# Optimization experiments

Hardware: AMD Instinct MI355X
Metric: run time of the kernel (lower is better)

Reference implementation:

```python
import jax, jax.numpy as jnp
from jax import lax
import numpy as np

B = 512
IN_CAPS, OUT_CAPS, IN_DIM, OUT_DIM, ITERS = 32 * 6 * 6, 10, 8, 16, 3
EPS = 1e-8


def setup_inputs() -> dict:
    key = jax.random.key(0)
    ks = jax.random.split(key, 12)
    inp = {
        "x": jax.random.normal(ks[0], (B, 1, 28, 28), dtype=jnp.float32),
        "conv1_w": jax.random.normal(ks[1], (256, 1, 9, 9), dtype=jnp.float32) * 0.05,
        "conv1_b": jnp.zeros((256,), dtype=jnp.float32),
        "conv2_w": jax.random.normal(ks[2], (256, 256, 9, 9), dtype=jnp.float32) * 0.02,
        "conv2_b": jnp.zeros((256,), dtype=jnp.float32),
        "W": jax.random.normal(ks[3], (IN_CAPS, OUT_CAPS, IN_DIM, OUT_DIM), dtype=jnp.float32) * 0.1,
        "d1_w": jax.random.normal(ks[4], (OUT_DIM * OUT_CAPS, 512), dtype=jnp.float32) * 0.05,
        "d1_b": jnp.zeros((512,), dtype=jnp.float32),
        "d2_w": jax.random.normal(ks[5], (512, 1024), dtype=jnp.float32) * 0.05,
        "d2_b": jnp.zeros((1024,), dtype=jnp.float32),
        "d3_w": jax.random.normal(ks[6], (1024, 28 * 28), dtype=jnp.float32) * 0.05,
        "d3_b": jnp.zeros((28 * 28,), dtype=jnp.float32),
    }
    return inp


def _squash(s):
    # s2/(1+s2) * s/sqrt(s2+eps), norm over last dim
    s2 = jnp.sum(s * s, axis=-1, keepdims=True)
    return s2 / (1.0 + s2) * (s / jnp.sqrt(s2 + EPS))


def _conv(x, w, b, stride):
    y = lax.conv_general_dilated(x, w, (stride, stride), "VALID",
                                 dimension_numbers=("NCHW", "OIHW", "NCHW"))
    return y + b[None, :, None, None]


def reference(x, conv1_w, conv1_b, conv2_w, conv2_b, W,
              d1_w, d1_b, d2_w, d2_b, d3_w, d3_b):
    h = jax.nn.relu(_conv(x, conv1_w, conv1_b, 1))          # [B,256,20,20]
    h = _conv(h, conv2_w, conv2_b, 2)                       # [B,256,6,6]
    u = h.reshape(h.shape[0], 8, IN_CAPS).transpose(0, 2, 1)  # [B,1152,8]
    u = _squash(u)

    # dynamic routing
    u_hat = jnp.einsum("ijnm,bin->bijm", W, u)              # [B,1152,10,16]
    b_log = jnp.zeros((u.shape[0], IN_CAPS, OUT_CAPS), dtype=u.dtype)
    v = None
    for _ in range(ITERS):
        c = jax.nn.softmax(b_log, axis=1)                   # over in_capsules (as original)
        s = jnp.einsum("bij,bijm->bjm", c, u_hat)           # [B,10,16]
        v = _squash(s)
        b_log = b_log + jnp.einsum("bjm,bijm->bij", v, u_hat)
    caps = v                                                # [B,10,16]

    pred = jnp.argmax(jnp.sum(caps * caps, axis=-1), axis=-1)  # [B]
    mask = jax.lax.stop_gradient(jax.nn.one_hot(pred, OUT_CAPS, dtype=caps.dtype))
    dec_in = (caps * mask[:, :, None]).reshape(caps.shape[0], -1)  # [B,160]
    r = jax.nn.relu(dec_in @ d1_w + d1_b)
    r = jax.nn.relu(r @ d2_w + d2_b)
    r = jax.nn.sigmoid(r @ d3_w + d3_b)
    recon = r.reshape(-1, 1, 28, 28)
    return caps, recon, pred
```

## Files before the change

kernel.cpp:

```cpp
#include <hip/hip_runtime.h>

#define CAPS_EPS 1e-8f

typedef __attribute__((ext_vector_type(8))) short short8;
typedef __attribute__((ext_vector_type(4))) float f32x4;

__device__ inline ushort bf16_rn(float f) {
    uint u = __float_as_uint(f);
    u += 0x7fff + ((u >> 16) & 1);
    return (ushort)(u >> 16);
}
__device__ inline float bf16_f(ushort h) { return __uint_as_float((uint)h << 16); }

__device__ __forceinline__ void gld16(const void* g, void* l) {
    __builtin_amdgcn_global_load_lds(
        (const __attribute__((address_space(1))) unsigned int*)g,
        (__attribute__((address_space(3))) unsigned int*)l, 16, 0, 0);
}


__global__ __launch_bounds__(256) void k_pre(const float* __restrict__ w2,
                                             ushort* __restrict__ wBhi,
                                             ushort* __restrict__ wBlo,
                                             const float* __restrict__ x,
                                             ushort* __restrict__ xhi,
                                             ushort* __restrict__ xlo,
                                             const float* __restrict__ w1,
                                             ushort* __restrict__ w1phi,
                                             ushort* __restrict__ w1plo) {
    int bx = blockIdx.x, tid = threadIdx.x;
    if (bx < 256) {
        __shared__ float ld[81 * 65];
        int n = bx;
        const float* src = w2 + (size_t)n * 20736;
        for (int cc = 0; cc < 4; ++cc) {
            for (int i = tid; i < 5184; i += 256) {
                int c_loc = i / 81, t = i - c_loc * 81;
                ld[t * 65 + c_loc] = src[cc * 5184 + i];
            }
            __syncthreads();
            for (int i = tid; i < 5184; i += 256) {
                int t = i >> 6, c_loc = i & 63;
                float f = ld[t * 65 + c_loc];
                ushort hi = bf16_rn(f);
                ushort lo = bf16_rn(f - bf16_f(hi));
                size_t o = (size_t)n * 20736 + t * 256 + cc * 64 + c_loc;
                wBhi[o] = hi;
                wBlo[o] = lo;
            }
            __syncthreads();
        }
    } else if (bx < 256 + 1569) {
        int idx = (bx - 256) * 256 + tid;
        if (idx < 401408) {
            float f = x[idx];
            ushort hi = bf16_rn(f);
            ushort lo = bf16_rn(f - bf16_f(hi));
            xhi[idx] = hi;
            xlo[idx] = lo;
        } else if (idx < 401472) {
            xhi[idx] = 0;
            xlo[idx] = 0;
        }
    } else {
        int idx = (bx - 1825) * 256 + tid;
        int c = idx / 160;
        int kk160 = idx - c * 160;
        int kstep = kk160 >> 5, kk = kk160 & 31;
        int ky = kstep * 2 + (kk >> 4), kx = kk & 15;
        float f = (ky < 9 && kx < 9) ? w1[c * 81 + ky * 9 + kx] : 0.f;
        ushort hi = bf16_rn(f);
        ushort lo = bf16_rn(f - bf16_f(hi));
        w1phi[idx] = hi;
        w1plo[idx] = lo;
    }
}

__global__ __launch_bounds__(256) void k_conv1m(const ushort* __restrict__ xhi,
                                                const ushort* __restrict__ xlo,
                                                const ushort* __restrict__ w1phi,
                                                const ushort* __restrict__ w1plo,
                                                const float* __restrict__ b1,
                                                ushort* __restrict__ h1hi,
                                                ushort* __restrict__ h1lo) {
    int tid = threadIdx.x;
    int wv = tid >> 6, lane = tid & 63;
    int lrow = lane & 15, quad = lane >> 4;
    int m0 = blockIdx.x * 128 + wv * 32;
    int c0 = blockIdx.y * 64;

    int am[2];
#pragma unroll
    for (int t = 0; t < 2; ++t) {
        int m = m0 + t * 16 + lrow;
        int b = m / 400, r = m - b * 400;
        int y = r / 20, xx = r - y * 20;
        am[t] = b * 784 + y * 28 + xx;
    }

    f32x4 acc[2][4];
#pragma unroll
    for (int t = 0; t < 2; ++t)
#pragma unroll
        for (int tn = 0; tn < 4; ++tn) acc[t][tn] = (f32x4){0.f, 0.f, 0.f, 0.f};

    for (int kstep = 0; kstep < 5; ++kstep) {
        int arow = (kstep * 2 + (quad >> 1)) * 28 + (quad & 1) * 8;
        int boff = kstep * 32 + quad * 8;
        short8 bh[4], bl2[4];
#pragma unroll
        for (int tn = 0; tn < 4; ++tn) {
            int br = (c0 + tn * 16 + lrow) * 160 + boff;
            bh[tn] = *reinterpret_cast<const short8*>(w1phi + br);
            bl2[tn] = *reinterpret_cast<const short8*>(w1plo + br);
        }
#pragma unroll
        for (int t = 0; t < 2; ++t) {
            short8 ah = *reinterpret_cast<const short8*>(xhi + am[t] + arow);
            short8 al = *reinterpret_cast<const short8*>(xlo + am[t] + arow);
#pragma unroll
            for (int tn = 0; tn < 4; ++tn) {
                acc[t][tn] = __builtin_amdgcn_mfma_f32_16x16x32_bf16(ah, bh[tn], acc[t][tn], 0, 0, 0);
                acc[t][tn] = __builtin_amdgcn_mfma_f32_16x16x32_bf16(ah, bl2[tn], acc[t][tn], 0, 0, 0);
                acc[t][tn] = __builtin_amdgcn_mfma_f32_16x16x32_bf16(al, bh[tn], acc[t][tn], 0, 0, 0);
            }
        }
    }

#pragma unroll
    for (int t = 0; t < 2; ++t)
#pragma unroll
        for (int r = 0; r < 4; ++r) {
            int m = m0 + t * 16 + quad * 4 + r;
#pragma unroll
            for (int tn = 0; tn < 4; ++tn) {
                int c = c0 + tn * 16 + lrow;
                float v = acc[t][tn][r] + b1[c];
                v = fmaxf(v, 0.f);
                ushort hi = bf16_rn(v);
                ushort lo = bf16_rn(v - bf16_f(hi));
                h1hi[(size_t)m * 256 + c] = hi;
                h1lo[(size_t)m * 256 + c] = lo;
            }
        }
}

__global__ __launch_bounds__(256) void k_h2init4(const float* __restrict__ b2,
                                                 float* __restrict__ h2) {
    size_t idx = (size_t)blockIdx.x * 256 + threadIdx.x;
    const float4* b24 = reinterpret_cast<const float4*>(b2);
    reinterpret_cast<float4*>(h2)[idx] = b24[idx & 63];
}

__global__ __launch_bounds__(256, 2) void k_conv2m(const ushort* __restrict__ h1hi,
                                                   const ushort* __restrict__ h1lo,
                                                   const ushort* __restrict__ wBhi,
                                                   const ushort* __restrict__ wBlo,
                                                   float* __restrict__ h2) {
    __shared__ ushort Ahi[128 * 32];
    __shared__ ushort Alo[128 * 32];
    __shared__ ushort Bhi[256 * 32];
    __shared__ ushort Blo[256 * 32];
    int tid = threadIdx.x;
    int m0 = blockIdx.y * 128;
    int kbase = blockIdx.x * 2592;

    int wv = tid >> 6, lane = tid & 63;
    int cq = (lane & 3) * 8;

    int ra = wv * 32 + (lane >> 2);
    int mA0 = m0 + ra, mA1 = mA0 + 16;
    int mb0 = mA0 / 36, mp0 = mA0 - mb0 * 36;
    int mb1 = mA1 / 36, mp1 = mA1 - mb1 * 36;
    size_t a0 = ((size_t)mb0 * 400 + (mp0 / 6) * 40 + (mp0 % 6) * 2) * 256 + cq;
    size_t a1 = ((size_t)mb1 * 400 + (mp1 / 6) * 40 + (mp1 % 6) * 2) * 256 + cq;
    int ldsA = wv * 1024;

    int rb = wv * 64 + (lane >> 2);
    size_t bB = (size_t)rb * 20736 + cq;
    int ldsB = wv * 2048;

    int mhalf = (wv >> 1) * 64, nhalf = (wv & 1) * 128;
    int lrow = lane & 15, quad = lane >> 4;

    f32x4 acc[4][8];
#pragma unroll
    for (int a = 0; a < 4; ++a)
#pragma unroll
        for (int bq = 0; bq < 8; ++bq) acc[a][bq] = (f32x4){0.f, 0.f, 0.f, 0.f};

    for (int ks = 0; ks < 81; ++ks) {
        int k = kbase + ks * 32;
        int t = k >> 8, cc = k & 255;
        int ky = t / 9, kx = t - ky * 9;
        size_t koffA = (size_t)(ky * 5120 + kx * 256 + cc);

        __syncthreads();
        gld16(h1hi + a0 + koffA, &Ahi[ldsA]);
        gld16(h1hi + a1 + koffA, &Ahi[ldsA + 512]);
        gld16(h1lo + a0 + koffA, &Alo[ldsA]);
        gld16(h1lo + a1 + koffA, &Alo[ldsA + 512]);
#pragma unroll
        for (int q = 0; q < 4; ++q) {
            size_t bo = bB + (size_t)q * 331776 + k;
            gld16(wBhi + bo, &Bhi[ldsB + q * 512]);
            gld16(wBlo + bo, &Blo[ldsB + q * 512]);
        }
        __syncthreads();

        short8 ah[4], al[4];
#pragma unroll
        for (int tm = 0; tm < 4; ++tm) {
            int off = (mhalf + tm * 16 + lrow) * 32 + quad * 8;
            ah[tm] = *reinterpret_cast<short8*>(&Ahi[off]);
            al[tm] = *reinterpret_cast<short8*>(&Alo[off]);
        }
#pragma unroll
        for (int tn = 0; tn < 8; ++tn) {
            int off = (nhalf + tn * 16 + lrow) * 32 + quad * 8;
            short8 bh = *reinterpret_cast<short8*>(&Bhi[off]);
            short8 bl2 = *reinterpret_cast<short8*>(&Blo[off]);
#pragma unroll
            for (int tm = 0; tm < 4; ++tm) {
                acc[tm][tn] = __builtin_amdgcn_mfma_f32_16x16x32_bf16(ah[tm], bh, acc[tm][tn], 0, 0, 0);
                acc[tm][tn] = __builtin_amdgcn_mfma_f32_16x16x32_bf16(ah[tm], bl2, acc[tm][tn], 0, 0, 0);
                acc[tm][tn] = __builtin_amdgcn_mfma_f32_16x16x32_bf16(al[tm], bh, acc[tm][tn], 0, 0, 0);
            }
        }
    }

#pragma unroll
    for (int tm = 0; tm < 4; ++tm) {
        int mrow = m0 + mhalf + tm * 16 + quad * 4;
#pragma unroll
        for (int tn = 0; tn < 8; ++tn) {
            int ncol = nhalf + tn * 16 + lrow;
#pragma unroll
            for (int r = 0; r < 4; ++r)
                atomicAdd(&h2[(size_t)(mrow + r) * 256 + ncol], acc[tm][tn][r]);
        }
    }
}

__device__ __forceinline__ void wtrans(const float* __restrict__ src,
                                       ushort* __restrict__ dh,
                                       ushort* __restrict__ dl,
                                       float* ld, int kt, int nt, int K, int N,
                                       int tid) {
    for (int i = tid; i < 4096; i += 256) {
        int kk = i >> 6, nn = i & 63;
        int k = kt * 64 + kk, n = nt * 64 + nn;
        float f = (k < K && n < N) ? src[(size_t)k * N + n] : 0.f;
        ld[kk * 65 + nn] = f;
    }
    __syncthreads();
    for (int i = tid; i < 4096; i += 256) {
        int nn = i >> 6, kk = i & 63;
        int k = kt * 64 + kk, n = nt * 64 + nn;
        if (k < K) {
            float f = ld[kk * 65 + nn];
            ushort hi = bf16_rn(f);
            ushort lo = bf16_rn(f - bf16_f(hi));
            dh[(size_t)n * K + k] = hi;
            dl[(size_t)n * K + k] = lo;
        }
    }
}

__global__ __launch_bounds__(256) void k_post(const float* __restrict__ h2,
                                              float* __restrict__ uT,
                                              float* __restrict__ zr,
                                              const float* __restrict__ d1w,
                                              const float* __restrict__ d2w,
                                              const float* __restrict__ d3w,
                                              ushort* __restrict__ d1wThi, ushort* __restrict__ d1wTlo,
                                              ushort* __restrict__ d2wThi, ushort* __restrict__ d2wTlo,
                                              ushort* __restrict__ d3wThi, ushort* __restrict__ d3wTlo) {
    __shared__ float smem[8224 + 1056];
    int bx = blockIdx.x, t = threadIdx.x;
    if (bx < 576) {
        float (*ld)[257] = (float (*)[257])smem;
        float (*scl)[33] = (float (*)[33])(smem + 8224);
        int s = bx % 36;
        int b0 = (bx / 36) * 32;
        for (int bb = 0; bb < 32; ++bb)
            ld[bb][t] = h2[((size_t)(b0 + bb) * 36 + s) * 256 + t];
        __syncthreads();
        int b = t & 31, gb = (t >> 5) * 4;
#pragma unroll
        for (int q = 0; q < 4; ++q) {
            int g = gb + q;
            float s2 = 0.f;
#pragma unroll
            for (int n = 0; n < 8; ++n) {
                float vv = ld[b][g + n * 32];
                s2 = fmaf(vv, vv, s2);
            }
            scl[b][g] = s2 / ((1.f + s2) * sqrtf(s2 + CAPS_EPS));
        }
        __syncthreads();
        int hf = t >> 5;
        for (int gg = 0; gg < 32; ++gg) {
            int idx = hf * 32 + gg;
            int g = idx >> 3, n = idx & 7;
            uT[(((size_t)g * 36 + s) * 8 + n) * 512 + b0 + b] = ld[b][g + n * 32] * scl[b][g];
        }
    } else if (bx < 6421) {
        reinterpret_cast<float4*>(zr)[(size_t)(bx - 576) * 256 + t] = make_float4(0, 0, 0, 0);
    } else if (bx < 6445) {
        int local = bx - 6421;
        wtrans(d1w, d1wThi, d1wTlo, smem, local / 8, local % 8, 160, 512, t);
    } else if (bx < 6573) {
        int local = bx - 6445;
        wtrans(d2w, d2wThi, d2wTlo, smem, local / 16, local % 16, 512, 1024, t);
    } else {
        int local = bx - 6573;
        wtrans(d3w, d3wThi, d3wTlo, smem, local / 14, local % 14, 1024, 784, t);
    }
}

__global__ __launch_bounds__(256) void k_s(const float* __restrict__ Wc,
                                           const float* __restrict__ uT,
                                           const float* __restrict__ bl,
                                           const float* __restrict__ Z,
                                           float* __restrict__ sT,
                                           int first) {
    __shared__ float lw[8 * 1280];
    int tid = threadIdx.x;
    int i0 = blockIdx.x * 8;
    int b = blockIdx.y * 128 + (tid & 127);
    int mh = tid >> 7;
    const float* wg = Wc + (size_t)i0 * 1280;
#pragma unroll
    for (int r = 0; r < 10; ++r) {
        int q4 = (r * 256 + tid) * 4;
        *reinterpret_cast<float4*>(&lw[q4]) = *reinterpret_cast<const float4*>(wg + q4);
    }
    __syncthreads();
    float rzs[10];
    if (!first) {
#pragma unroll
        for (int j = 0; j < 10; ++j) rzs[j] = 1.0f / Z[j * 512 + b];
    }
    float acc[80];
#pragma unroll
    for (int q = 0; q < 80; ++q) acc[q] = 0.f;
    for (int di = 0; di < 8; ++di) {
        int i = i0 + di;
        float ur[8];
#pragma unroll
        for (int n = 0; n < 8; ++n) ur[n] = uT[((size_t)i * 8 + n) * 512 + b];
#pragma unroll
        for (int j = 0; j < 10; ++j) {
            float c;
            if (first) c = (1.0f / 1152.0f);
            else c = expf(bl[((size_t)i * 10 + j) * 512 + b]) * rzs[j];
            const float* wp = &lw[(di * 10 + j) * 128 + mh * 8];
            float4 s0 = {0.f, 0.f, 0.f, 0.f}, s1 = {0.f, 0.f, 0.f, 0.f};
#pragma unroll
            for (int n = 0; n < 8; ++n) {
                const float4* wq = reinterpret_cast<const float4*>(wp + n * 16);
                float4 wa = wq[0], wb = wq[1];
                float un = ur[n];
                s0.x = fmaf(un, wa.x, s0.x); s0.y = fmaf(un, wa.y, s0.y);
                s0.z = fmaf(un, wa.z, s0.z); s0.w = fmaf(un, wa.w, s0.w);
                s1.x = fmaf(un, wb.x, s1.x); s1.y = fmaf(un, wb.y, s1.y);
                s1.z = fmaf(un, wb.z, s1.z); s1.w = fmaf(un, wb.w, s1.w);
            }
            acc[j * 8 + 0] = fmaf(c, s0.x, acc[j * 8 + 0]);
            acc[j * 8 + 1] = fmaf(c, s0.y, acc[j * 8 + 1]);
            acc[j * 8 + 2] = fmaf(c, s0.z, acc[j * 8 + 2]);
            acc[j * 8 + 3] = fmaf(c, s0.w, acc[j * 8 + 3]);
            acc[j * 8 + 4] = fmaf(c, s1.x, acc[j * 8 + 4]);
            acc[j * 8 + 5] = fmaf(c, s1.y, acc[j * 8 + 5]);
            acc[j * 8 + 6] = fmaf(c, s1.z, acc[j * 8 + 6]);
            acc[j * 8 + 7] = fmaf(c, s1.w, acc[j * 8 + 7]);
        }
    }
#pragma unroll
    for (int j = 0; j < 10; ++j)
#pragma unroll
        for (int mm = 0; mm < 8; ++mm)
            atomicAdd(&sT[(j * 16 + mh * 8 + mm) * 512 + b], acc[j * 8 + mm]);
}

__global__ __launch_bounds__(256) void k_v(const float* __restrict__ sT,
                                           float* __restrict__ v,
                                           float* __restrict__ vT,
                                           float* __restrict__ sTz,
                                           float* __restrict__ Z) {
    int idx = blockIdx.x * 256 + threadIdx.x;
    int j = idx >> 9;
    int b = idx & 511;
    float sv[16];
    float s2 = 0.f;
#pragma unroll
    for (int m = 0; m < 16; ++m) {
        sv[m] = sT[(j * 16 + m) * 512 + b];
        s2 = fmaf(sv[m], sv[m], s2);
    }
    float scale = s2 / ((1.f + s2) * sqrtf(s2 + CAPS_EPS));
#pragma unroll
    for (int m = 0; m < 16; ++m) {
        float val = sv[m] * scale;
        v[(size_t)b * 160 + j * 16 + m] = val;
        vT[(j * 16 + m) * 512 + b] = val;
        sTz[(j * 16 + m) * 512 + b] = 0.f;
    }
    Z[idx] = 0.f;
}

__global__ __launch_bounds__(256) void k_bupd(const float* __restrict__ Wc,
                                              const float* __restrict__ uT,
                                              const float* __restrict__ vT,
                                              float* __restrict__ bl,
                                              float* __restrict__ Z) {
    __shared__ float lw[8 * 1280];
    int tid = threadIdx.x;
    int i0 = blockIdx.x * 8;
    int b = blockIdx.y * 128 + (tid & 127);
    int ih = tid >> 7;
    const float* wg = Wc + (size_t)i0 * 1280;
#pragma unroll
    for (int r = 0; r < 10; ++r) {
        int q4 = (r * 256 + tid) * 4;
        *reinterpret_cast<float4*>(&lw[q4]) = *reinterpret_cast<const float4*>(wg + q4);
    }
    __syncthreads();
    float ur[4][8];
#pragma unroll
    for (int ii = 0; ii < 4; ++ii) {
        int i = i0 + ih * 4 + ii;
#pragma unroll
        for (int n = 0; n < 8; ++n) ur[ii][n] = uT[((size_t)i * 8 + n) * 512 + b];
    }
    for (int j = 0; j < 10; ++j) {
        float vj[16];
#pragma unroll
        for (int m = 0; m < 16; ++m) vj[m] = vT[(j * 16 + m) * 512 + b];
        float zp = 0.f;
#pragma unroll
        for (int ii = 0; ii < 4; ++ii) {
            int di = ih * 4 + ii;
            const float* wp = &lw[(di * 10 + j) * 128];
            float t = 0.f;
#pragma unroll
            for (int n = 0; n < 8; ++n) {
                const float4* wq = reinterpret_cast<const float4*>(wp + n * 16);
                float4 w0 = wq[0], w1 = wq[1], w2 = wq[2], w3 = wq[3];
                float wvv = w0.x * vj[0];
                wvv = fmaf(w0.y, vj[1], wvv);  wvv = fmaf(w0.z, vj[2], wvv);
                wvv = fmaf(w0.w, vj[3], wvv);  wvv = fmaf(w1.x, vj[4], wvv);
                wvv = fmaf(w1.y, vj[5], wvv);  wvv = fmaf(w1.z, vj[6], wvv);
                wvv = fmaf(w1.w, vj[7], wvv);  wvv = fmaf(w2.x, vj[8], wvv);
                wvv = fmaf(w2.y, vj[9], wvv);  wvv = fmaf(w2.z, vj[10], wvv);
                wvv = fmaf(w2.w, vj[11], wvv); wvv = fmaf(w3.x, vj[12], wvv);
                wvv = fmaf(w3.y, vj[13], wvv); wvv = fmaf(w3.z, vj[14], wvv);
                wvv = fmaf(w3.w, vj[15], wvv);
                t = fmaf(ur[ii][n], wvv, t);
            }
            size_t idx = ((size_t)(i0 + di) * 10 + j) * 512 + b;
            float nb = bl[idx] + t;
            bl[idx] = nb;
            zp += expf(nb);
        }
        atomicAdd(&Z[j * 512 + b], zp);
    }
}

__global__ __launch_bounds__(256) void k_pred(const float* __restrict__ v,
                                              float* __restrict__ out,
                                              ushort* __restrict__ dechi,
                                              ushort* __restrict__ declo,
                                              int pred_off) {
    int b = blockIdx.x, t = threadIdx.x;
    __shared__ float sq[160];
    __shared__ float nrm[10];
    __shared__ int ip;
    float val = 0.f;
    if (t < 160) {
        val = v[(size_t)b * 160 + t];
        out[(size_t)b * 160 + t] = val;
        sq[t] = val * val;
    }
    __syncthreads();
    if (t < 10) {
        float s = 0.f;
#pragma unroll
        for (int k = 0; k < 16; ++k) s += sq[t * 16 + k];
        nrm[t] = s;
    }
    __syncthreads();
    if (t == 0) {
        float best = nrm[0];
        int bi = 0;
        for (int j = 1; j < 10; ++j)
            if (nrm[j] > best) { best = nrm[j]; bi = j; }
        ip = bi;
        out[(size_t)pred_off + b] = (float)bi;
    }
    __syncthreads();
    if (t < 160) {
        float d = ((t >> 4) == ip) ? val : 0.f;
        ushort hi = bf16_rn(d);
        ushort lo = bf16_rn(d - bf16_f(hi));
        dechi[(size_t)b * 160 + t] = hi;
        declo[(size_t)b * 160 + t] = lo;
    }
}

template <int ACT, int SPLIT_OUT>
__global__ __launch_bounds__(256) void k_gemmm(const ushort* __restrict__ Ahi,
                                               const ushort* __restrict__ Alo,
                                               const ushort* __restrict__ Bhi,
                                               const ushort* __restrict__ Blo,
                                               const float* __restrict__ bias,
                                               ushort* __restrict__ Chi,
                                               ushort* __restrict__ Clo,
                                               float* __restrict__ Cf,
                                               int K, int Ng) {
    int tid = threadIdx.x;
    int wv = tid >> 6, lane = tid & 63;
    int lrow = lane & 15, quad = lane >> 4;
    int m0 = blockIdx.x * 64 + (wv >> 1) * 32;
    int n0 = blockIdx.y * 128 + (wv & 1) * 64;

    f32x4 acc[2][4];
#pragma unroll
    for (int t = 0; t < 2; ++t)
#pragma unroll
        for (int tn = 0; tn < 4; ++tn) acc[t][tn] = (f32x4){0.f, 0.f, 0.f, 0.f};

    for (int ks = 0; ks < K; ks += 32) {
        int boff = ks + quad * 8;
        short8 bh[4], bl2[4];
#pragma unroll
        for (int tn = 0; tn < 4; ++tn) {
            size_t br = (size_t)(n0 + tn * 16 + lrow) * K + boff;
            bh[tn] = *reinterpret_cast<const short8*>(Bhi + br);
            bl2[tn] = *reinterpret_cast<const short8*>(Blo + br);
        }
#pragma unroll
        for (int t = 0; t < 2; ++t) {
            size_t ar = (size_t)(m0 + t * 16 + lrow) * K + boff;
            short8 ah = *reinterpret_cast<const short8*>(Ahi + ar);
            short8 al = *reinterpret_cast<const short8*>(Alo + ar);
#pragma unroll
            for (int tn = 0; tn < 4; ++tn) {
                acc[t][tn] = __builtin_amdgcn_mfma_f32_16x16x32_bf16(ah, bh[tn], acc[t][tn], 0, 0, 0);
                acc[t][tn] = __builtin_amdgcn_mfma_f32_16x16x32_bf16(ah, bl2[tn], acc[t][tn], 0, 0, 0);
                acc[t][tn] = __builtin_amdgcn_mfma_f32_16x16x32_bf16(al, bh[tn], acc[t][tn], 0, 0, 0);
            }
        }
    }

#pragma unroll
    for (int t = 0; t < 2; ++t)
#pragma unroll
        for (int r = 0; r < 4; ++r) {
            int m = m0 + t * 16 + quad * 4 + r;
#pragma unroll
            for (int tn = 0; tn < 4; ++tn) {
                int n = n0 + tn * 16 + lrow;
                if (n < Ng) {
                    float val = acc[t][tn][r] + bias[n];
                    if (ACT == 0) val = fmaxf(val, 0.f);
                    else val = 1.f / (1.f + expf(-val));
                    if (SPLIT_OUT) {
                        ushort hi = bf16_rn(val);
                        ushort lo = bf16_rn(val - bf16_f(hi));
                        Chi[(size_t)m * Ng + n] = hi;
                        Clo[(size_t)m * Ng + n] = lo;
                    } else {
                        Cf[(size_t)m * Ng + n] = val;
                    }
                }
            }
        }
}

extern "C" void kernel_launch(void* const* d_in, const int* in_sizes, int n_in,
                              void* d_out, int out_size, void* d_ws, size_t ws_size,
                              hipStream_t stream) {
    const float* x   = (const float*)d_in[0];
    const float* w1  = (const float*)d_in[1];
    const float* b1  = (const float*)d_in[2];
    const float* w2  = (const float*)d_in[3];
    const float* b2  = (const float*)d_in[4];
    const float* Wc  = (const float*)d_in[5];
    const float* d1w = (const float*)d_in[6];
    const float* d1b = (const float*)d_in[7];
    const float* d2w = (const float*)d_in[8];
    const float* d2b = (const float*)d_in[9];
    const float* d3w = (const float*)d_in[10];
    const float* d3b = (const float*)d_in[11];
    float* out = (float*)d_out;

    ushort* wBhi = (ushort*)d_ws;
    ushort* wBlo = wBhi + 5308416;
    ushort* h1hi = (ushort*)((char*)d_ws + 21233664);
    ushort* h1lo = h1hi + 52428800;
    char*   h2b  = (char*)d_ws + 230948864;
    float*  h2   = (float*)h2b;
    ushort* xhi   = (ushort*)h2b;
    ushort* xlo   = xhi + 401472;
    ushort* w1phi = xlo + 401472;
    ushort* w1plo = w1phi + 40960;

    float* post = (float*)((char*)d_ws + 21233664);
    float* uT  = post + 4718592;
    float* bl  = post + 9437184;
    float* sT  = post + 15335424;
    float* Z   = post + 15417344;
    float* v   = post + 15422464;
    float* vT  = post + 15504384;
    ushort* ub = (ushort*)(post + 15586304);
    ushort* dechi   = ub;
    ushort* declo   = ub + 81920;
    ushort* r1hi    = ub + 163840;
    ushort* r1lo    = ub + 425984;
    ushort* r2hi    = ub + 688128;
    ushort* r2lo    = ub + 1212416;
    ushort* d1wThi  = ub + 1736704;
    ushort* d1wTlo  = ub + 1818624;
    ushort* d2wThi  = ub + 1900544;
    ushort* d2wTlo  = ub + 2424832;
    ushort* d3wThi  = ub + 2949120;
    ushort* d3wTlo  = ub + 3866624;

    int pred_off = out_size - 512;

    k_pre<<<1985, 256, 0, stream>>>(w2, wBhi, wBlo, x, xhi, xlo, w1, w1phi, w1plo);
    k_conv1m<<<dim3(1600, 4), 256, 0, stream>>>(xhi, xlo, w1phi, w1plo, b1, h1hi, h1lo);
    k_h2init4<<<4608, 256, 0, stream>>>(b2, h2);
    k_conv2m<<<dim3(8, 144), 256, 0, stream>>>(h1hi, h1lo, wBhi, wBlo, h2);
    k_post<<<6797, 256, 0, stream>>>(h2, uT, bl, d1w, d2w, d3w,
                                     d1wThi, d1wTlo, d2wThi, d2wTlo, d3wThi, d3wTlo);

    for (int it = 0; it < 3; ++it) {
        k_s<<<dim3(144, 4), 256, 0, stream>>>(Wc, uT, bl, Z, sT, it == 0 ? 1 : 0);
        k_v<<<20, 256, 0, stream>>>(sT, v, vT, sT, Z);
        if (it < 2) k_bupd<<<dim3(144, 4), 256, 0, stream>>>(Wc, uT, vT, bl, Z);
    }

    k_pred<<<512, 256, 0, stream>>>(v, out, dechi, declo, pred_off);
    k_gemmm<0, 1><<<dim3(8, 4), 256, 0, stream>>>(dechi, declo, d1wThi, d1wTlo, d1b,
                                                  r1hi, r1lo, nullptr, 160, 512);
    k_gemmm<0, 1><<<dim3(8, 8), 256, 0, stream>>>(r1hi, r1lo, d2wThi, d2wTlo, d2b,
                                                  r2hi, r2lo, nullptr, 512, 1024);
    k_gemmm<1, 0><<<dim3(8, 7), 256, 0, stream>>>(r2hi, r2lo, d3wThi, d3wTlo, d3b,
                                                  nullptr, nullptr, out + 81920, 1024, 784);
}
```

Measured before the change: 1.372 ms.

## Stream conv2 low-part activations from global, raise occupancy, fold routing normalization

In conv2, the low bf16 half of the activations is no longer staged through LDS. Each lane now loads it straight from global memory into registers, which shrinks shared memory use and lets the launch bound ask for 3 blocks per SM instead of 2. The grid axes are also swapped so that neighbouring blocks share the same K slice of weights. In the routing part, the softmax division by Z moves out of k_s and into k_v, the loop is unrolled, and the last squash is fused into the prediction kernel (k_predv), removing one launch and the v round trip. The risk is that the direct global loads are uncached and poorly coalesced, and they add latency inside the MFMA loop.

Measured after the change: 2.044 ms. 49.1% more time.

```diff
diff --git a/kernel.cpp b/kernel.cpp
--- a/kernel.cpp
+++ b/kernel.cpp
@@ -152,18 +152,17 @@
     reinterpret_cast<float4*>(h2)[idx] = b24[idx & 63];
 }
 
-__global__ __launch_bounds__(256, 2) void k_conv2m(const ushort* __restrict__ h1hi,
+__global__ __launch_bounds__(256, 3) void k_conv2m(const ushort* __restrict__ h1hi,
                                                    const ushort* __restrict__ h1lo,
                                                    const ushort* __restrict__ wBhi,
                                                    const ushort* __restrict__ wBlo,
                                                    float* __restrict__ h2) {
     __shared__ ushort Ahi[128 * 32];
-    __shared__ ushort Alo[128 * 32];
     __shared__ ushort Bhi[256 * 32];
     __shared__ ushort Blo[256 * 32];
     int tid = threadIdx.x;
-    int m0 = blockIdx.y * 128;
-    int kbase = blockIdx.x * 2592;
+    int m0 = blockIdx.x * 128;
+    int kbase = blockIdx.y * 2592;
 
     int wv = tid >> 6, lane = tid & 63;
     int cq = (lane & 3) * 8;
@@ -183,6 +182,15 @@
     int mhalf = (wv >> 1) * 64, nhalf = (wv & 1) * 128;
     int lrow = lane & 15, quad = lane >> 4;
 
+    size_t aL[4];
+#pragma unroll
+    for (int tm = 0; tm < 4; ++tm) {
+        int m = m0 + mhalf + tm * 16 + lrow;
+        int b = m / 36, p = m - b * 36;
+        int oy = p / 6, ox = p - oy * 6;
+        aL[tm] = ((size_t)b * 400 + oy * 40 + ox * 2) * 256 + quad * 8;
+    }
+
     f32x4 acc[4][8];
 #pragma unroll
     for (int a = 0; a < 4; ++a)
@@ -198,8 +206,6 @@
         __syncthreads();
         gld16(h1hi + a0 + koffA, &Ahi[ldsA]);
         gld16(h1hi + a1 + koffA, &Ahi[ldsA + 512]);
-        gld16(h1lo + a0 + koffA, &Alo[ldsA]);
-        gld16(h1lo + a1 + koffA, &Alo[ldsA + 512]);
 #pragma unroll
         for (int q = 0; q < 4; ++q) {
             size_t bo = bB + (size_t)q * 331776 + k;
@@ -213,7 +219,7 @@
         for (int tm = 0; tm < 4; ++tm) {
             int off = (mhalf + tm * 16 + lrow) * 32 + quad * 8;
             ah[tm] = *reinterpret_cast<short8*>(&Ahi[off]);
-            al[tm] = *reinterpret_cast<short8*>(&Alo[off]);
+            al[tm] = *reinterpret_cast<const short8*>(h1lo + aL[tm] + koffA);
         }
 #pragma unroll
         for (int tn = 0; tn < 8; ++tn) {
@@ -322,7 +328,6 @@
 __global__ __launch_bounds__(256) void k_s(const float* __restrict__ Wc,
                                            const float* __restrict__ uT,
                                            const float* __restrict__ bl,
-                                           const float* __restrict__ Z,
                                            float* __restrict__ sT,
                                            int first) {
     __shared__ float lw[8 * 1280];
@@ -337,11 +342,6 @@
         *reinterpret_cast<float4*>(&lw[q4]) = *reinterpret_cast<const float4*>(wg + q4);
     }
     __syncthreads();
-    float rzs[10];
-    if (!first) {
-#pragma unroll
-        for (int j = 0; j < 10; ++j) rzs[j] = 1.0f / Z[j * 512 + b];
-    }
     float acc[80];
 #pragma unroll
     for (int q = 0; q < 80; ++q) acc[q] = 0.f;
@@ -353,8 +353,8 @@
 #pragma unroll
         for (int j = 0; j < 10; ++j) {
             float c;
-            if (first) c = (1.0f / 1152.0f);
-            else c = expf(bl[((size_t)i * 10 + j) * 512 + b]) * rzs[j];
+            if (first) c = 1.0f;
+            else c = expf(bl[((size_t)i * 10 + j) * 512 + b]);
             const float* wp = &lw[(di * 10 + j) * 128 + mh * 8];
             float4 s0 = {0.f, 0.f, 0.f, 0.f}, s1 = {0.f, 0.f, 0.f, 0.f};
 #pragma unroll
@@ -385,18 +385,21 @@
 }
 
 __global__ __launch_bounds__(256) void k_v(const float* __restrict__ sT,
+                                           const float* __restrict__ Z,
                                            float* __restrict__ v,
                                            float* __restrict__ vT,
                                            float* __restrict__ sTz,
-                                           float* __restrict__ Z) {
+                                           float* __restrict__ Zz,
+                                           int first) {
     int idx = blockIdx.x * 256 + threadIdx.x;
     int j = idx >> 9;
     int b = idx & 511;
+    float rz = first ? (1.0f / 1152.0f) : (1.0f / Z[j * 512 + b]);
     float sv[16];
     float s2 = 0.f;
 #pragma unroll
     for (int m = 0; m < 16; ++m) {
-        sv[m] = sT[(j * 16 + m) * 512 + b];
+        sv[m] = sT[(j * 16 + m) * 512 + b] * rz;
         s2 = fmaf(sv[m], sv[m], s2);
     }
     float scale = s2 / ((1.f + s2) * sqrtf(s2 + CAPS_EPS));
@@ -407,7 +410,7 @@
         vT[(j * 16 + m) * 512 + b] = val;
         sTz[(j * 16 + m) * 512 + b] = 0.f;
     }
-    Z[idx] = 0.f;
+    Zz[idx] = 0.f;
 }
 
 __global__ __launch_bounds__(256) void k_bupd(const float* __restrict__ Wc,
@@ -468,20 +471,23 @@
     }
 }
 
-__global__ __launch_bounds__(256) void k_pred(const float* __restrict__ v,
-                                              float* __restrict__ out,
-                                              ushort* __restrict__ dechi,
-                                              ushort* __restrict__ declo,
-                                              int pred_off) {
+__global__ __launch_bounds__(256) void k_predv(const float* __restrict__ sT,
+                                               const float* __restrict__ Z,
+                                               float* __restrict__ out,
+                                               ushort* __restrict__ dechi,
+                                               ushort* __restrict__ declo,
+                                               int pred_off) {
     int b = blockIdx.x, t = threadIdx.x;
     __shared__ float sq[160];
     __shared__ float nrm[10];
+    __shared__ float scl[10];
+    __shared__ float vnrm[10];
     __shared__ int ip;
-    float val = 0.f;
+    float raw = 0.f;
+    int j = t >> 4;
     if (t < 160) {
-        val = v[(size_t)b * 160 + t];
-        out[(size_t)b * 160 + t] = val;
-        sq[t] = val * val;
+        raw = sT[(size_t)t * 512 + b] / Z[j * 512 + b];
+        sq[t] = raw * raw;
     }
     __syncthreads();
     if (t < 10) {
@@ -489,19 +495,27 @@
 #pragma unroll
         for (int k = 0; k < 16; ++k) s += sq[t * 16 + k];
         nrm[t] = s;
+        float sc = s / ((1.f + s) * sqrtf(s + CAPS_EPS));
+        scl[t] = sc;
+        vnrm[t] = s * sc * sc;
     }
     __syncthreads();
+    float val = 0.f;
+    if (t < 160) {
+        val = raw * scl[j];
+        out[(size_t)b * 160 + t] = val;
+    }
     if (t == 0) {
-        float best = nrm[0];
+        float best = vnrm[0];
         int bi = 0;
-        for (int j = 1; j < 10; ++j)
-            if (nrm[j] > best) { best = nrm[j]; bi = j; }
+        for (int jj = 1; jj < 10; ++jj)
+            if (vnrm[jj] > best) { best = vnrm[jj]; bi = jj; }
         ip = bi;
         out[(size_t)pred_off + b] = (float)bi;
     }
     __syncthreads();
     if (t < 160) {
-        float d = ((t >> 4) == ip) ? val : 0.f;
+        float d = (j == ip) ? val : 0.f;
         ushort hi = bf16_rn(d);
         ushort lo = bf16_rn(d - bf16_f(hi));
         dechi[(size_t)b * 160 + t] = hi;
@@ -633,17 +647,19 @@
     k_pre<<<1985, 256, 0, stream>>>(w2, wBhi, wBlo, x, xhi, xlo, w1, w1phi, w1plo);
     k_conv1m<<<dim3(1600, 4), 256, 0, stream>>>(xhi, xlo, w1phi, w1plo, b1, h1hi, h1lo);
     k_h2init4<<<4608, 256, 0, stream>>>(b2, h2);
-    k_conv2m<<<dim3(8, 144), 256, 0, stream>>>(h1hi, h1lo, wBhi, wBlo, h2);
+    k_conv2m<<<dim3(144, 8), 256, 0, stream>>>(h1hi, h1lo, wBhi, wBlo, h2);
     k_post<<<6797, 256, 0, stream>>>(h2, uT, bl, d1w, d2w, d3w,
                                      d1wThi, d1wTlo, d2wThi, d2wTlo, d3wThi, d3wTlo);
 
-    for (int it = 0; it < 3; ++it) {
-        k_s<<<dim3(144, 4), 256, 0, stream>>>(Wc, uT, bl, Z, sT, it == 0 ? 1 : 0);
-        k_v<<<20, 256, 0, stream>>>(sT, v, vT, sT, Z);
-        if (it < 2) k_bupd<<<dim3(144, 4), 256, 0, stream>>>(Wc, uT, vT, bl, Z);
-    }
-
-    k_pred<<<512, 256, 0, stream>>>(v, out, dechi, declo, pred_off);
+    k_s<<<dim3(144, 4), 256, 0, stream>>>(Wc, uT, bl, sT, 1);
+    k_v<<<20, 256, 0, stream>>>(sT, Z, v, vT, sT, Z, 1);
+    k_bupd<<<dim3(144, 4), 256, 0, stream>>>(Wc, uT, vT, bl, Z);
+    k_s<<<dim3(144, 4), 256, 0, stream>>>(Wc, uT, bl, sT, 0);
+    k_v<<<20, 256, 0, stream>>>(sT, Z, v, vT, sT, Z, 0);
+    k_bupd<<<dim3(144, 4), 256, 0, stream>>>(Wc, uT, vT, bl, Z);
+    k_s<<<dim3(144, 4), 256, 0, stream>>>(Wc, uT, bl, sT, 0);
+    k_predv<<<512, 256, 0, stream>>>(sT, Z, out, dechi, declo, pred_off);
+
     k_gemmm<0, 1><<<dim3(8, 4), 256, 0, stream>>>(dechi, declo, d1wThi, d1wTlo, d1b,
                                                   r1hi, r1lo, nullptr, 160, 512);
     k_gemmm<0, 1><<<dim3(8, 8), 256, 0, stream>>>(r1hi, r1lo, d2wThi, d2wTlo, d2b,
```
